# Kernel optimization log

Hardware: AMD Instinct MI355X
Metric: run time of the kernel (lower is better)

The kernel has to match this reference:

```python
import jax, jax.numpy as jnp
import numpy as np

EMBED_DIM = 1024
ATTN_DIM = 1024
BATCH = 4
SEQ = 2048


def setup_inputs() -> dict:
    key = jax.random.key(0)
    k1, k2, k3, k4 = jax.random.split(key, 4)
    embedded = jax.random.normal(k1, (BATCH, SEQ, EMBED_DIM), dtype=jnp.float32)
    # torch Linear weights have shape [out_features, in_features]
    scale = 1.0 / np.sqrt(EMBED_DIM)
    W_K = jax.random.uniform(k2, (ATTN_DIM, EMBED_DIM), dtype=jnp.float32, minval=-scale, maxval=scale)
    W_Q = jax.random.uniform(k3, (ATTN_DIM, EMBED_DIM), dtype=jnp.float32, minval=-scale, maxval=scale)
    W_V = jax.random.uniform(k4, (ATTN_DIM, EMBED_DIM), dtype=jnp.float32, minval=-scale, maxval=scale)
    return {"embedded": embedded, "W_K": W_K, "W_Q": W_Q, "W_V": W_V}


def reference(embedded, W_K, W_Q, W_V):
    # embedded: [B, L, E]; W_*: [A, E] (torch Linear layout, applied as x @ W.T)
    L = embedded.shape[1]
    A = W_K.shape[0]
    K = jnp.einsum('ble,ae->bla', embedded, W_K)
    Q = jnp.einsum('ble,ae->bla', embedded, W_Q)
    V = jnp.einsum('ble,ae->bla', embedded, W_V)
    att = jnp.einsum('bqa,bka->bqk', Q, K) / jnp.sqrt(jnp.float32(A))  # [B, L, L]
    causal = jnp.tril(jnp.ones((L, L), dtype=bool))  # lower-triangular mask
    att = jnp.where(causal, att, -jnp.inf)
    att = jax.nn.softmax(att, axis=-1)
    return jnp.einsum('bqk,bka->bqa', att, V)
```

## Files before the change

### kernel.cpp

```cpp
#include <hip/hip_runtime.h>
#include <hip/hip_bf16.h>
#include <stdint.h>

#define BATCH 4
#define SEQ   2048
#define EMB   1024
#define ADIM  1024

typedef __attribute__((ext_vector_type(8))) short  short8;
typedef __attribute__((ext_vector_type(4))) float  float4v;

static __device__ __forceinline__ unsigned short f2bf(float f) {
    unsigned int u = __float_as_uint(f);
    u += 0x7FFFu + ((u >> 16) & 1u);
    return (unsigned short)(u >> 16);
}

static __device__ __forceinline__ uint2 pack4(float4v v) {
    uint2 r;
    r.x = (unsigned)f2bf(v.x) | ((unsigned)f2bf(v.y) << 16);
    r.y = (unsigned)f2bf(v.z) | ((unsigned)f2bf(v.w) << 16);
    return r;
}

static __device__ __forceinline__ void gload16(const void* g, void* l) {
    __builtin_amdgcn_global_load_lds(
        (const __attribute__((address_space(1))) void*)g,
        (__attribute__((address_space(3))) void*)l, 16, 0, 0);
}

static __device__ __forceinline__ int swz8(int row) { return ((row >> 1) & 3) << 3; }

__global__ __launch_bounds__(256) void prep_kernel(
    const float* __restrict__ X,  const float* __restrict__ Wv,
    const float* __restrict__ Wq, const float* __restrict__ Wk,
    unsigned short* __restrict__ Xb, unsigned short* __restrict__ Wvb,
    unsigned short* __restrict__ WqT, unsigned short* __restrict__ WkT,
    float* __restrict__ rowsum, float* __restrict__ out)
{
    __shared__ unsigned short T[64][72];
    const int bI = blockIdx.x;
    if (bI < 4608) {
        const float* src; unsigned short* dst; int off;
        if (bI < 4096) { src = X;  dst = Xb;  off = bI; }
        else           { src = Wv; dst = Wvb; off = bI - 4096; }
        const int i = (off * 256 + threadIdx.x) * 8;
        float4v a = *(const float4v*)(src + i);
        float4v b = *(const float4v*)(src + i + 4);
        uint2 pa = pack4(a), pb = pack4(b);
        uint4 o; o.x = pa.x; o.y = pa.y; o.z = pb.x; o.w = pb.y;
        *(uint4*)(dst + i) = o;
        return;
    }
    if (bI < 4616) {
        const int i = ((bI - 4608) * 256 + threadIdx.x) * 4;
        *(float4v*)(rowsum + i) = float4v{0.f, 0.f, 0.f, 0.f};
        return;
    }
    if (bI >= 5128) {
        const int o   = bI - 5128;
        const int b   = o >> 10;
        const int blk = o & 1023;
        float* dst = out + ((size_t)(b * 2048 + 1024) * 1024)
                         + (size_t)blk * 1024 + threadIdx.x * 4;
        *(float4v*)dst = float4v{0.f, 0.f, 0.f, 0.f};
        return;
    }
    const int z    = (bI - 4616) >> 8;
    const int tile = (bI - 4616) & 255;
    const int ti = tile >> 4;
    const int tj = tile & 15;
    const float* W = z ? Wk : Wq;
    unsigned short* WT = z ? WkT : WqT;
    const int t  = threadIdx.x;
    const int r  = t >> 2;
    const int c  = (t & 3) << 4;

    const float* src = W + (size_t)(ti * 64 + r) * EMB + tj * 64 + c;
    #pragma unroll
    for (int u = 0; u < 4; ++u) {
        float4v v = *(const float4v*)(src + 4 * u);
        uint2 p = pack4(v);
        *(uint2*)&T[r][c + 4 * u] = p;
    }
    __syncthreads();
    unsigned short tmp[16];
    #pragma unroll
    for (int u = 0; u < 16; ++u) tmp[u] = T[c + u][r];
    unsigned short* dst = WT + (size_t)(tj * 64 + r) * EMB + ti * 64 + c;
    *(uint4*)(dst)     = *(uint4*)&tmp[0];
    *(uint4*)(dst + 8) = *(uint4*)&tmp[8];
}

static __device__ __forceinline__ void gemm_core(
    const unsigned short* __restrict__ A, const unsigned short* __restrict__ B,
    int lda, int ldb, int m0, int n0, int klen,
    unsigned short* As, unsigned short* Bs, float4v acc[4][4])
{
    const int tid  = threadIdx.x;
    const int r    = tid >> 2;
    const int c8   = ((tid & 3) << 3) ^ swz8(tid >> 2);
    const int lane = tid & 63;
    const int wave = tid >> 6;
    const int quad = lane >> 4;
    const int l16  = lane & 15;
    const int wm   = (wave >> 1) << 6;
    const int wn   = (wave & 1) << 6;

    const unsigned short* Ag = A + (size_t)(m0 + r) * lda + c8;
    const unsigned short* Bg = B + (size_t)(n0 + r) * ldb + c8;
    unsigned short* Al = As + tid * 8;
    unsigned short* Bl = Bs + tid * 8;
    const int niter = klen >> 5;

    #define ISSUE_A(k0, st) do { \
        unsigned short* al_ = Al + (st) * 4096; \
        gload16(Ag + (k0),                    al_); \
        gload16(Ag + (k0) + (size_t)64 * lda, al_ + 2048); \
    } while (0)
    #define ISSUE_B(k0, st) do { \
        unsigned short* bl_ = Bl + (st) * 4096; \
        gload16(Bg + (k0),                    bl_); \
        gload16(Bg + (k0) + (size_t)64 * ldb, bl_ + 2048); \
    } while (0)

    ISSUE_A(0, 0);  ISSUE_B(0, 0);
    ISSUE_A(32, 1); ISSUE_B(32, 1);

    int ci = 0, ii = 2;
    for (int it = 0; it < niter; ++it) {
        const int knext = (it + 2 < niter) ? ((it + 2) << 5) : 0;
        const unsigned short* Ah = As + ci * 4096;
        const unsigned short* Bh = Bs + ci * 4096;
        short8 bfr[4];

        ISSUE_A(knext, ii);
        asm volatile("s_waitcnt vmcnt(6)" ::: "memory");
        asm volatile("s_barrier" ::: "memory");
        {
            short8 af0, af1;
            {
                const int row = wm + l16;
                af0 = *(const short8*)&Ah[row * 32 + ((quad * 8) ^ swz8(row))];
            }
            {
                const int row = wm + 16 + l16;
                af1 = *(const short8*)&Ah[row * 32 + ((quad * 8) ^ swz8(row))];
            }
            #pragma unroll
            for (int j = 0; j < 4; ++j) {
                const int row = wn + 16 * j + l16;
                bfr[j] = *(const short8*)&Bh[row * 32 + ((quad * 8) ^ swz8(row))];
            }
            __builtin_amdgcn_s_setprio(1);
            #pragma unroll
            for (int j = 0; j < 4; ++j)
                acc[0][j] = __builtin_amdgcn_mfma_f32_16x16x32_bf16(af0, bfr[j], acc[0][j], 0, 0, 0);
            #pragma unroll
            for (int j = 0; j < 4; ++j)
                acc[1][j] = __builtin_amdgcn_mfma_f32_16x16x32_bf16(af1, bfr[j], acc[1][j], 0, 0, 0);
            __builtin_amdgcn_s_setprio(0);
        }
        asm volatile("s_barrier" ::: "memory");

        ISSUE_B(knext, ii);
        {
            short8 af2, af3;
            {
                const int row = wm + 32 + l16;
                af2 = *(const short8*)&Ah[row * 32 + ((quad * 8) ^ swz8(row))];
            }
            {
                const int row = wm + 48 + l16;
                af3 = *(const short8*)&Ah[row * 32 + ((quad * 8) ^ swz8(row))];
            }
            __builtin_amdgcn_s_setprio(1);
            #pragma unroll
            for (int j = 0; j < 4; ++j)
                acc[2][j] = __builtin_amdgcn_mfma_f32_16x16x32_bf16(af2, bfr[j], acc[2][j], 0, 0, 0);
            #pragma unroll
            for (int j = 0; j < 4; ++j)
                acc[3][j] = __builtin_amdgcn_mfma_f32_16x16x32_bf16(af3, bfr[j], acc[3][j], 0, 0, 0);
            __builtin_amdgcn_s_setprio(0);
        }
        asm volatile("s_barrier" ::: "memory");
        ci = (ci == 2) ? 0 : ci + 1;
        ii = (ii == 2) ? 0 : ii + 1;
    }
    asm volatile("s_waitcnt vmcnt(0)" ::: "memory");
    #undef ISSUE_A
    #undef ISSUE_B
}

#define DECL_TILE_IDX() \
    const int lane = threadIdx.x & 63; \
    const int wave = threadIdx.x >> 6; \
    const int quad = lane >> 4; \
    const int l16  = lane & 15; \
    const int wm   = (wave >> 1) << 6; \
    const int wn   = (wave & 1) << 6;

__global__ __launch_bounds__(256, 3) void m_kernel(
    const unsigned short* __restrict__ WkT, const unsigned short* __restrict__ WqT,
    float* __restrict__ Mtf)
{
    __shared__ __align__(16) unsigned short As[3 * 128 * 32];
    __shared__ __align__(16) unsigned short Bs[3 * 128 * 32];
    const int idx = blockIdx.x;
    const int kc  = idx >> 6;
    const int t   = idx & 63;
    const int m0  = (t >> 3) << 7;
    const int n0  = (t & 7) << 7;

    float4v acc[4][4];
    #pragma unroll
    for (int i = 0; i < 4; ++i)
        #pragma unroll
        for (int j = 0; j < 4; ++j)
            acc[i][j] = float4v{0.f, 0.f, 0.f, 0.f};

    gemm_core(WkT + kc * 256, WqT + kc * 256, EMB, EMB, m0, n0, 256, As, Bs, acc);

    float* dst = Mtf + (size_t)kc * 1024 * 1024;
    DECL_TILE_IDX();
    #pragma unroll
    for (int i = 0; i < 4; ++i)
        #pragma unroll
        for (int j = 0; j < 4; ++j)
            #pragma unroll
            for (int rr = 0; rr < 4; ++rr) {
                const int row = m0 + wm + 16 * i + quad * 4 + rr;
                const int col = n0 + wn + 16 * j + l16;
                dst[(size_t)row * EMB + col] = acc[i][j][rr];
            }
}

__global__ __launch_bounds__(256) void mc_kernel(
    const float* __restrict__ Mtf, unsigned short* __restrict__ Mt)
{
    const int base = (blockIdx.x * 256 + threadIdx.x) * 16;
    #pragma unroll
    for (int u = 0; u < 4; ++u) {
        const int i = base + u * 4;
        float4v s = *(const float4v*)(Mtf + i);
        s = s + *(const float4v*)(Mtf + 1048576 + i);
        s = s + *(const float4v*)(Mtf + 2097152 + i);
        s = s + *(const float4v*)(Mtf + 3145728 + i);
        s = s * 0.03125f;
        uint2 p = pack4(s);
        *(uint2*)(Mt + i) = p;
    }
}

__global__ __launch_bounds__(512, 2) void qv_kernel(
    const unsigned short* __restrict__ Xb, const unsigned short* __restrict__ Mt,
    const unsigned short* __restrict__ Wvb,
    unsigned short* __restrict__ Qpb, unsigned short* __restrict__ Vtb)
{
    __shared__ __align__(16) unsigned short LDS[49152];
    unsigned short* As = LDS;
    unsigned short* Bs = LDS + 24576;

    const int idx  = blockIdx.x;
    const int mt   = ((idx & 7) << 2) | ((idx >> 3) & 3);
    const int slot = idx >> 5;
    const int z    = slot >> 2;
    const int n0   = (slot & 3) << 8;
    const int m0   = mt << 8;
    const unsigned short* B = z ? Wvb : Mt;

    const int tid  = threadIdx.x;
    const int lane = tid & 63;
    const int wave = tid >> 6;
    const int quad = lane >> 4;
    const int l16  = lane & 15;
    const int wm   = (wave >> 2) << 7;
    const int wn   = (wave & 3) << 6;

    const int srow = tid >> 2;
    const int c8   = ((tid & 3) << 3) ^ swz8(srow);

    const unsigned short* Ag0 = Xb + (size_t)(m0 + srow) * EMB + c8;
    const unsigned short* Ag1 = Ag0 + (size_t)128 * EMB;
    const unsigned short* Bg0 = B  + (size_t)(n0 + srow) * EMB + c8;
    const unsigned short* Bg1 = Bg0 + (size_t)128 * EMB;
    unsigned short* Al = As + tid * 8;
    unsigned short* Bl = Bs + tid * 8;

    #define ISSUE_QA(t, st) do { \
        gload16(Ag0 + (t) * 32, Al + (st) * 8192); \
        gload16(Ag1 + (t) * 32, Al + (st) * 8192 + 4096); \
    } while (0)
    #define ISSUE_QB(t, st) do { \
        gload16(Bg0 + (t) * 32, Bl + (st) * 8192); \
        gload16(Bg1 + (t) * 32, Bl + (st) * 8192 + 4096); \
    } while (0)

    float4v acc[8][4];
    #pragma unroll
    for (int i = 0; i < 8; ++i)
        #pragma unroll
        for (int j = 0; j < 4; ++j)
            acc[i][j] = float4v{0.f, 0.f, 0.f, 0.f};

    ISSUE_QA(0, 0); ISSUE_QB(0, 0);
    ISSUE_QA(1, 1); ISSUE_QB(1, 1);

    int ci = 0, ii = 2;
    for (int it = 0; it < 32; ++it) {
        const int tn = (it + 2 < 32) ? (it + 2) : 0;
        const unsigned short* Ah = As + ci * 8192;
        const unsigned short* Bh = Bs + ci * 8192;
        short8 bfr[4];

        ISSUE_QA(tn, ii);
        asm volatile("s_waitcnt vmcnt(6)" ::: "memory");
        asm volatile("s_barrier" ::: "memory");
        {
            short8 af[4];
            #pragma unroll
            for (int i = 0; i < 4; ++i) {
                const int row = wm + 16 * i + l16;
                af[i] = *(const short8*)&Ah[row * 32 + ((quad * 8) ^ swz8(row))];
            }
            #pragma unroll
            for (int j = 0; j < 4; ++j) {
                const int row = wn + 16 * j + l16;
                bfr[j] = *(const short8*)&Bh[row * 32 + ((quad * 8) ^ swz8(row))];
            }
            __builtin_amdgcn_s_setprio(1);
            #pragma unroll
            for (int i = 0; i < 4; ++i)
                #pragma unroll
                for (int j = 0; j < 4; ++j)
                    acc[i][j] = __builtin_amdgcn_mfma_f32_16x16x32_bf16(af[i], bfr[j], acc[i][j], 0, 0, 0);
            __builtin_amdgcn_s_setprio(0);
        }
        asm volatile("s_barrier" ::: "memory");

        ISSUE_QB(tn, ii);
        {
            short8 af[4];
            #pragma unroll
            for (int i = 0; i < 4; ++i) {
                const int row = wm + 64 + 16 * i + l16;
                af[i] = *(const short8*)&Ah[row * 32 + ((quad * 8) ^ swz8(row))];
            }
            __builtin_amdgcn_s_setprio(1);
            #pragma unroll
            for (int i = 0; i < 4; ++i)
                #pragma unroll
                for (int j = 0; j < 4; ++j)
                    acc[i + 4][j] = __builtin_amdgcn_mfma_f32_16x16x32_bf16(af[i], bfr[j], acc[i + 4][j], 0, 0, 0);
            __builtin_amdgcn_s_setprio(0);
        }
        asm volatile("s_barrier" ::: "memory");
        ci = (ci == 2) ? 0 : ci + 1;
        ii = (ii == 2) ? 0 : ii + 1;
    }
    asm volatile("s_waitcnt vmcnt(0)" ::: "memory");
    #undef ISSUE_QA
    #undef ISSUE_QB

    if (z == 0) {
        #pragma unroll
        for (int i = 0; i < 8; ++i)
            #pragma unroll
            for (int j = 0; j < 4; ++j)
                #pragma unroll
                for (int rr = 0; rr < 4; ++rr) {
                    const int row = m0 + wm + ((i & 3) << 4) + ((i >> 2) << 6) + quad * 4 + rr;
                    const int col = n0 + wn + 16 * j + l16;
                    Qpb[(size_t)row * ADIM + col] = f2bf(acc[i][j][rr]);
                }
    } else {
        const int bb = m0 >> 11;
        const int l0 = m0 & (SEQ - 1);
        #pragma unroll
        for (int h = 0; h < 2; ++h) {
            __syncthreads();
            if ((wm >> 7) == h) {
                #pragma unroll
                for (int i = 0; i < 8; ++i)
                    #pragma unroll
                    for (int j = 0; j < 4; ++j) {
                        const int qloc = ((i & 3) << 4) + ((i >> 2) << 6) + quad * 4;
                        const int acol = wn + 16 * j + l16;
                        uint2 w;
                        w.x = (unsigned)f2bf(acc[i][j][0]) | ((unsigned)f2bf(acc[i][j][1]) << 16);
                        w.y = (unsigned)f2bf(acc[i][j][2]) | ((unsigned)f2bf(acc[i][j][3]) << 16);
                        *(uint2*)&LDS[acol * 136 + qloc] = w;
                    }
            }
            __syncthreads();
            const int acol = tid >> 1;
            const int qh   = (tid & 1) << 6;
            unsigned short* dst = Vtb + (((size_t)(bb * ADIM + n0 + acol)) << 11)
                                      + l0 + h * 128 + qh;
            #pragma unroll
            for (int u = 0; u < 8; ++u)
                *(uint4*)(dst + u * 8) = *(const uint4*)&LDS[acol * 136 + qh + u * 8];
        }
    }
}

__global__ __launch_bounds__(256, 3) void s_kernel(
    const unsigned short* __restrict__ Qpb, const unsigned short* __restrict__ Xb,
    unsigned short* __restrict__ E, float* __restrict__ rowsum)
{
    const int idx = blockIdx.x;
    const int x   = idx & 7;
    const int j   = idx >> 3;
    const int b   = j / 17;
    const int u   = j - b * 17;
    const int qt  = (u <= x) ? x : 15 - x;
    const int kt  = (u <= x) ? u : u - (x + 1);
    const int q0  = qt << 7;
    const int k0  = kt << 7;

    __shared__ __align__(16) unsigned short As[3 * 128 * 32];
    __shared__ __align__(16) unsigned short Bs[3 * 128 * 32];

    float4v acc[4][4];
    #pragma unroll
    for (int i = 0; i < 4; ++i)
        #pragma unroll
        for (int jj = 0; jj < 4; ++jj)
            acc[i][jj] = float4v{0.f, 0.f, 0.f, 0.f};

    gemm_core(Qpb + (size_t)b * SEQ * ADIM, Xb + (size_t)b * SEQ * EMB,
              ADIM, EMB, q0, k0, EMB, As, Bs, acc);

    unsigned short* Eb = E + (size_t)b * SEQ * SEQ;
    float* rsb = rowsum + (size_t)b * SEQ;
    DECL_TILE_IDX();
    #pragma unroll
    for (int i = 0; i < 4; ++i)
        #pragma unroll
        for (int rr = 0; rr < 4; ++rr) {
            const int row = q0 + wm + 16 * i + quad * 4 + rr;
            float s = 0.f;
            #pragma unroll
            for (int jj = 0; jj < 4; ++jj) {
                const int col = k0 + wn + 16 * jj + l16;
                float e = (col <= row) ? __expf(acc[i][jj][rr]) : 0.f;
                s += e;
                Eb[(size_t)row * SEQ + col] = f2bf(e);
            }
            s += __shfl_xor(s, 1);
            s += __shfl_xor(s, 2);
            s += __shfl_xor(s, 4);
            s += __shfl_xor(s, 8);
            if (l16 == 0) atomicAdd(&rsb[row], s);
        }
}

__global__ __launch_bounds__(256, 3) void pv_kernel(
    const unsigned short* __restrict__ E, const unsigned short* __restrict__ Vtb,
    const float* __restrict__ rowsum, float* __restrict__ out)
{
    const int idx  = blockIdx.x;
    const int x    = idx & 7;
    const int j    = idx >> 3;
    const int slot = j >> 5;
    const int c    = j & 31;
    const int b    = c >> 3;
    const int a0   = (c & 7) << 7;

    int qt, kbeg, klen, dual;
    if (slot == 0)      { qt = x;      kbeg = 0;    klen = (x + 1) << 7; dual = 0; }
    else if (slot == 1) { qt = 15 - x; kbeg = 0;    klen = 1024;         dual = 1; }
    else                { qt = 15 - x; kbeg = 1024; klen = (8 - x) << 7; dual = 1; }
    const int q0 = qt << 7;

    __shared__ __align__(16) unsigned short As[3 * 128 * 32];
    __shared__ __align__(16) unsigned short Bs[3 * 128 * 32];

    float4v acc[4][4];
    #pragma unroll
    for (int i = 0; i < 4; ++i)
        #pragma unroll
        for (int jj = 0; jj < 4; ++jj)
            acc[i][jj] = float4v{0.f, 0.f, 0.f, 0.f};

    gemm_core(E + (size_t)b * SEQ * SEQ + kbeg, Vtb + (size_t)b * ADIM * SEQ + kbeg,
              SEQ, SEQ, q0, a0, klen, As, Bs, acc);

    float* ob = out + (size_t)b * SEQ * ADIM;
    const float* rsb = rowsum + (size_t)b * SEQ;
    DECL_TILE_IDX();
    if (!dual) {
        #pragma unroll
        for (int i = 0; i < 4; ++i)
            #pragma unroll
            for (int rr = 0; rr < 4; ++rr) {
                const int row = q0 + wm + 16 * i + quad * 4 + rr;
                const float inv = 1.0f / rsb[row];
                #pragma unroll
                for (int jj = 0; jj < 4; ++jj) {
                    const int col = a0 + wn + 16 * jj + l16;
                    ob[(size_t)row * ADIM + col] = acc[i][jj][rr] * inv;
                }
            }
    } else {
        #pragma unroll
        for (int i = 0; i < 4; ++i)
            #pragma unroll
            for (int rr = 0; rr < 4; ++rr) {
                const int row = q0 + wm + 16 * i + quad * 4 + rr;
                const float inv = 1.0f / rsb[row];
                #pragma unroll
                for (int jj = 0; jj < 4; ++jj) {
                    const int col = a0 + wn + 16 * jj + l16;
                    atomicAdd(&ob[(size_t)row * ADIM + col], acc[i][jj][rr] * inv);
                }
            }
    }
}

extern "C" void kernel_launch(void* const* d_in, const int* in_sizes, int n_in,
                              void* d_out, int out_size, void* d_ws, size_t ws_size,
                              hipStream_t stream)
{
    const float* X  = (const float*)d_in[0];
    const float* Wk = (const float*)d_in[1];
    const float* Wq = (const float*)d_in[2];
    const float* Wv = (const float*)d_in[3];
    float* out = (float*)d_out;

    const size_t MB = 1024 * 1024;
    char* ws = (char*)d_ws;
    unsigned short* Xb  = (unsigned short*)(ws);
    unsigned short* Wvb = (unsigned short*)(ws + 16 * MB);
    unsigned short* WqT = (unsigned short*)(ws + 18 * MB);
    unsigned short* WkT = (unsigned short*)(ws + 20 * MB);
    unsigned short* Mt  = (unsigned short*)(ws + 22 * MB);
    unsigned short* Qpb = (unsigned short*)(ws + 24 * MB);
    unsigned short* E   = (unsigned short*)(ws + 40 * MB);
    unsigned short* Vtb = (unsigned short*)(ws + 72 * MB);
    float*          rowsum = (float*)(ws + 88 * MB);
    float*          Mtf = (float*)(ws + 40 * MB);

    hipLaunchKernelGGL(prep_kernel, dim3(9224), dim3(256), 0, stream,
                       X, Wv, Wq, Wk, Xb, Wvb, WqT, WkT, rowsum, out);
    hipLaunchKernelGGL(m_kernel, dim3(256), dim3(256), 0, stream, WkT, WqT, Mtf);
    hipLaunchKernelGGL(mc_kernel, dim3(256), dim3(256), 0, stream, Mtf, Mt);
    hipLaunchKernelGGL(qv_kernel, dim3(256), dim3(512), 0, stream,
                       Xb, Mt, Wvb, Qpb, Vtb);
    hipLaunchKernelGGL(s_kernel, dim3(544), dim3(256), 0, stream, Qpb, Xb, E, rowsum);
    hipLaunchKernelGGL(pv_kernel, dim3(768), dim3(256), 0, stream, E, Vtb, rowsum, out);
}
```

Baseline: 231.2 us.

## Balance PV kernel work by splitting paired query-tile K ranges evenly

The PV kernel now treats each pair of query tiles (x and 15-x) as one combined run of 68 K-chunks and splits it evenly across three blocks, so every block does about the same work. Before, one slot handled only the short diagonal tile and the other two slots split the long tile unevenly. Because every block may now write a partial result, all output rows use atomic adds, and the prep kernel zeroes the whole output instead of only the second half. This costs more atomic traffic and an extra zeroing pass over the output in exchange for removing load imbalance.

```diff
diff --git a/kernel.cpp b/kernel.cpp
--- a/kernel.cpp
+++ b/kernel.cpp
@@ -59,10 +59,9 @@
     }
     if (bI >= 5128) {
         const int o   = bI - 5128;
-        const int b   = o >> 10;
-        const int blk = o & 1023;
-        float* dst = out + ((size_t)(b * 2048 + 1024) * 1024)
-                         + (size_t)blk * 1024 + threadIdx.x * 4;
+        const int b   = o >> 11;
+        const int row = o & 2047;
+        float* dst = out + ((size_t)(b * 2048 + row) * 1024) + threadIdx.x * 4;
         *(float4v*)dst = float4v{0.f, 0.f, 0.f, 0.f};
         return;
     }
@@ -459,37 +458,48 @@
     const unsigned short* __restrict__ E, const unsigned short* __restrict__ Vtb,
     const float* __restrict__ rowsum, float* __restrict__ out)
 {
-    const int idx  = blockIdx.x;
-    const int x    = idx & 7;
-    const int j    = idx >> 3;
-    const int slot = j >> 5;
-    const int c    = j & 31;
-    const int b    = c >> 3;
-    const int a0   = (c & 7) << 7;
-
-    int qt, kbeg, klen, dual;
-    if (slot == 0)      { qt = x;      kbeg = 0;    klen = (x + 1) << 7; dual = 0; }
-    else if (slot == 1) { qt = 15 - x; kbeg = 0;    klen = 1024;         dual = 1; }
-    else                { qt = 15 - x; kbeg = 1024; klen = (8 - x) << 7; dual = 1; }
-    const int q0 = qt << 7;
+    const int idx = blockIdx.x;
+    const int x   = idx & 7;
+    const int j   = idx >> 3;
+    const int c   = j >> 5;
+    const int col = j & 31;
+    const int b   = col >> 3;
+    const int a0  = (col & 7) << 7;
+
+    const int ea  = (x + 1) << 2;
+    const int g0  = (c == 0) ? 0 : ((c == 1) ? 23 : 46);
+    const int g1  = (c == 2) ? 68 : (g0 + 23);
 
     __shared__ __align__(16) unsigned short As[3 * 128 * 32];
     __shared__ __align__(16) unsigned short Bs[3 * 128 * 32];
 
-    float4v acc[4][4];
-    #pragma unroll
-    for (int i = 0; i < 4; ++i)
-        #pragma unroll
-        for (int jj = 0; jj < 4; ++jj)
-            acc[i][jj] = float4v{0.f, 0.f, 0.f, 0.f};
-
-    gemm_core(E + (size_t)b * SEQ * SEQ + kbeg, Vtb + (size_t)b * ADIM * SEQ + kbeg,
-              SEQ, SEQ, q0, a0, klen, As, Bs, acc);
-
+    const unsigned short* Eb = E   + (size_t)b * SEQ * SEQ;
+    const unsigned short* Vb = Vtb + (size_t)b * ADIM * SEQ;
     float* ob = out + (size_t)b * SEQ * ADIM;
     const float* rsb = rowsum + (size_t)b * SEQ;
     DECL_TILE_IDX();
-    if (!dual) {
+
+    #pragma unroll
+    for (int seg = 0; seg < 2; ++seg) {
+        const int lo = seg ? ea : 0;
+        const int hi = seg ? 68 : ea;
+        const int s0 = (g0 > lo) ? g0 : lo;
+        const int s1 = (g1 < hi) ? g1 : hi;
+        if (s0 >= s1) continue;
+        const int qt   = seg ? (15 - x) : x;
+        const int q0   = qt << 7;
+        const int kbeg = (s0 - lo) << 5;
+        const int klen = (s1 - s0) << 5;
+
+        float4v acc[4][4];
+        #pragma unroll
+        for (int i = 0; i < 4; ++i)
+            #pragma unroll
+            for (int jj = 0; jj < 4; ++jj)
+                acc[i][jj] = float4v{0.f, 0.f, 0.f, 0.f};
+
+        gemm_core(Eb + kbeg, Vb + kbeg, SEQ, SEQ, q0, a0, klen, As, Bs, acc);
+
         #pragma unroll
         for (int i = 0; i < 4; ++i)
             #pragma unroll
@@ -498,23 +508,11 @@
                 const float inv = 1.0f / rsb[row];
                 #pragma unroll
                 for (int jj = 0; jj < 4; ++jj) {
-                    const int col = a0 + wn + 16 * jj + l16;
-                    ob[(size_t)row * ADIM + col] = acc[i][jj][rr] * inv;
+                    const int col2 = a0 + wn + 16 * jj + l16;
+                    atomicAdd(&ob[(size_t)row * ADIM + col2], acc[i][jj][rr] * inv);
                 }
             }
-    } else {
-        #pragma unroll
-        for (int i = 0; i < 4; ++i)
-            #pragma unroll
-            for (int rr = 0; rr < 4; ++rr) {
-                const int row = q0 + wm + 16 * i + quad * 4 + rr;
-                const float inv = 1.0f / rsb[row];
-                #pragma unroll
-                for (int jj = 0; jj < 4; ++jj) {
-                    const int col = a0 + wn + 16 * jj + l16;
-                    atomicAdd(&ob[(size_t)row * ADIM + col], acc[i][jj][rr] * inv);
-                }
-            }
+        __syncthreads();
     }
 }
 
@@ -541,7 +539,7 @@
     float*          rowsum = (float*)(ws + 88 * MB);
     float*          Mtf = (float*)(ws + 40 * MB);
 
-    hipLaunchKernelGGL(prep_kernel, dim3(9224), dim3(256), 0, stream,
+    hipLaunchKernelGGL(prep_kernel, dim3(13320), dim3(256), 0, stream,
                        X, Wv, Wq, Wk, Xb, Wvb, WqT, WkT, rowsum, out);
     hipLaunchKernelGGL(m_kernel, dim3(256), dim3(256), 0, stream, WkT, WqT, Mtf);
     hipLaunchKernelGGL(mc_kernel, dim3(256), dim3(256), 0, stream, Mtf, Mt);
```

Result: slower. 254.0 us (+9.9%).
